# Kernel tuning notes

Hardware: AMD Instinct MI355X
Metric: run time of the kernel (lower is better)

Reference implementation:

```python
import jax, jax.numpy as jnp
import numpy as np
from jax import lax

KERNEL = 3
NUM_ITERS = 10
SMOOTH = 1.0


def _max_pool3d(x):
    # x: (B, 1, Z, Y, X); 3x3x3 max pool, stride 1, SAME padding
    return lax.reduce_window(
        x, -jnp.inf, lax.max,
        window_dimensions=(1, 1, KERNEL, KERNEL, KERNEL),
        window_strides=(1, 1, 1, 1, 1),
        padding='SAME')


def _soft_erode(x):
    return -_max_pool3d(-x)


def _soft_dilate(x):
    return _max_pool3d(x)


def _soft_open(x):
    return _soft_dilate(_soft_erode(x))


def _soft_skeletonize(img):
    skel = jax.nn.relu(img - _soft_open(img))
    for _ in range(NUM_ITERS):
        img = _soft_erode(img)
        delta = jax.nn.relu(img - _soft_open(img))
        skel = skel + jax.nn.relu(delta - skel * delta)
    return skel


def setup_inputs() -> dict:
    key = jax.random.key(0)
    k1, k2 = jax.random.split(key)
    B, C, Z, Y, X = 2, 2, 192, 192, 192
    logits = jax.random.normal(k1, (B, C, Z, Y, X), dtype=jnp.float32)
    targets = jax.random.randint(k2, (B, Z, Y, X), 0, 2, dtype=jnp.int32)
    return {"logits": logits, "targets": targets}


def reference(logits, targets):
    probs = jax.nn.softmax(logits, axis=1)
    pred_surface = probs[:, 1:2]                                  # (B,1,Z,Y,X)
    gt_surface = (targets == 1).astype(jnp.float32)[:, None]      # (B,1,Z,Y,X)
    skel_pred = _soft_skeletonize(pred_surface)
    skel_gt = _soft_skeletonize(gt_surface)
    tprec = (jnp.sum(skel_pred * gt_surface) + SMOOTH) / (jnp.sum(skel_pred) + SMOOTH)
    tsens = (jnp.sum(skel_gt * pred_surface) + SMOOTH) / (jnp.sum(skel_gt) + SMOOTH)
    cl_dice = 2.0 * tprec * tsens / (tprec + tsens + 1e-07)
    return 1.0 - cl_dice
```

## Files before the change

### kernel.cpp

```cpp
#include <hip/hip_runtime.h>
#include <hip/hip_fp16.h>


#define ZD 192
#define YD 192
#define XD 192
constexpr int PLANE = YD * XD;
constexpr int VOL   = ZD * PLANE;
constexpr int NVOL4 = 4 * VOL;

constexpr int XT = 64, YT = 16, ZCH = 16;
constexpr int IWQ = 18, SIW = 19;
constexpr int IH  = 20;
constexpr int NIMGQ = IH * IWQ;
constexpr int BWQ = 17, BH = 18;
constexpr int NBQ  = BH * BWQ;
constexpr int STEPS = ZCH + 4;
#define PINF __builtin_inff()

typedef _Float16 hv2 __attribute__((ext_vector_type(2)));
struct __align__(8) H4 { hv2 lo, hi; };

__device__ __forceinline__ unsigned h2u(hv2 h) { return __builtin_bit_cast(unsigned, h); }
__device__ __forceinline__ hv2 u2h(unsigned u) { return __builtin_bit_cast(hv2, u); }

__device__ __forceinline__ hv2 h2min(hv2 a, hv2 b) {
#if __has_builtin(__builtin_elementwise_min)
    return __builtin_elementwise_min(a, b);
#else
    unsigned r, ua = h2u(a), ub = h2u(b);
    asm("v_pk_min_f16 %0, %1, %2" : "=v"(r) : "v"(ua), "v"(ub));
    return u2h(r);
#endif
}
__device__ __forceinline__ hv2 h2max(hv2 a, hv2 b) {
#if __has_builtin(__builtin_elementwise_max)
    return __builtin_elementwise_max(a, b);
#else
    unsigned r, ua = h2u(a), ub = h2u(b);
    asm("v_pk_max_f16 %0, %1, %2" : "=v"(r) : "v"(ua), "v"(ub));
    return u2h(r);
#endif
}
__device__ __forceinline__ hv2 shf1(hv2 c, hv2 n) {
    return u2h(__builtin_amdgcn_alignbit(h2u(n), h2u(c), 16));
}
__device__ __forceinline__ H4 h4min(H4 a, H4 b) { H4 r; r.lo = h2min(a.lo, b.lo); r.hi = h2min(a.hi, b.hi); return r; }
__device__ __forceinline__ H4 h4max(H4 a, H4 b) { H4 r; r.lo = h2max(a.lo, b.lo); r.hi = h2max(a.hi, b.hi); return r; }
__device__ __forceinline__ H4 pk4(float4 v) {
    H4 r;
    r.lo.x = (_Float16)v.x; r.lo.y = (_Float16)v.y;
    r.hi.x = (_Float16)v.z; r.hi.y = (_Float16)v.w;
    return r;
}
__device__ __forceinline__ H4 ldp4(const __half* p) {
    const uint2 v = *(const uint2*)p;
    H4 r; r.lo = u2h(v.x); r.hi = u2h(v.y); return r;
}
__device__ __forceinline__ void stp4(__half* p, H4 v) {
    uint2 u; u.x = h2u(v.lo); u.y = h2u(v.hi);
    *(uint2*)p = u;
}
__device__ __forceinline__ void sth4(__half* p, float4 v) { stp4(p, pk4(v)); }

template <int MODE>
__global__ __launch_bounds__(256)
void fused_kernel(const __half* __restrict__ a_in,
                  __half* __restrict__ a_out,
                  __half* __restrict__ skel,
                  const float* __restrict__ logits,
                  const int* __restrict__ targets,
                  float* __restrict__ sums)
{
    __shared__ __align__(16) hv2 simg[2][IH * SIW * 2];
    __shared__ __align__(16) hv2 sbp[NBQ * 2 + 4];
    __shared__ float red[4][2];

    const int tx = threadIdx.x, ty = threadIdx.y;
    const int tid = ty * 16 + tx;
    const int x0 = (blockIdx.x % 3) * XT, y0 = (blockIdx.x / 3) * YT;
    const int z0 = blockIdx.y * ZCH;
    const int zf = blockIdx.z;
    const int bb = zf & 1, field = zf >> 1;
    const size_t voff = (size_t)zf * VOL;
    const __half* inb  = a_in  + voff;
    __half*       outb = a_out + voff;
    __half*       skb  = skel  + voff;
    const float* lg0 = logits + (size_t)(bb * 2) * VOL;
    const float* lg1 = lg0 + VOL;
    const int*   tgb = targets + (size_t)bb * VOL;

    const hv2 INF2  = u2h(0x7C007C00u);
    const hv2 NINF2 = u2h(0xFC00FC00u);
    const hv2 Z2    = u2h(0u);
    const H4 HINF4  = { INF2, INF2 };
    const H4 HNINF4 = { NINF2, NINF2 };
    const H4 HZ4    = { Z2, Z2 };

    const int q1off = ((tid & 3) << 6) + (tid >> 2);

    int im_qi[2] = { tid, 256 + q1off };
    int im_addr[2], im_goff[2]; bool im_ok[2], im_has[2];
    #pragma unroll
    for (int j = 0; j < 2; ++j) {
        const int qi = im_qi[j];
        const int r = qi / IWQ, c = qi - r * IWQ;
        const int gy = y0 - 2 + r, gxb = x0 - 4 + 4 * c;
        im_has[j] = (qi < NIMGQ);
        im_ok[j]  = im_has[j] && gy >= 0 && gy < YD && gxb >= 0 && gxb < XD;
        im_goff[j] = gy * XD + gxb;
        im_addr[j] = (r * SIW + c) * 2;
    }
    int bqi[2], brow[2], bcol[2]; bool bhas[2]; H4 bmask[2];
    #pragma unroll
    for (int j = 0; j < 2; ++j) {
        const int qi = (j == 0) ? tid : 256 + q1off;
        bqi[j] = qi;
        bhas[j] = (qi < NBQ);
        const int r = qi / BWQ, c = qi - r * BWQ;
        brow[j] = r; bcol[j] = c;
        const int gy = y0 - 1 + r, gxb = x0 - 1 + 4 * c;
        const bool yv = (gy >= 0 && gy < YD);
        float4 m;
        m.x = (yv && gxb     >= 0 && gxb     < XD) ? PINF : -PINF;
        m.y = (yv && gxb + 1 >= 0 && gxb + 1 < XD) ? PINF : -PINF;
        m.z = (yv && gxb + 2 >= 0 && gxb + 2 < XD) ? PINF : -PINF;
        m.w = (yv && gxb + 3 >= 0 && gxb + 3 < XD) ? PINF : -PINF;
        bmask[j] = pk4(m);
    }

    auto loadq = [&](int zi, int j) -> H4 {
        if (zi < 0 || zi >= ZD || !im_ok[j]) return HINF4;
        const size_t p = (size_t)zi * PLANE + im_goff[j];
        if constexpr (MODE == 0) {
            if (field) {
                const int4 t = *(const int4*)(tgb + p);
                return pk4(make_float4(t.x == 1 ? 1.f : 0.f, t.y == 1 ? 1.f : 0.f,
                                       t.z == 1 ? 1.f : 0.f, t.w == 1 ? 1.f : 0.f));
            } else {
                const float4 a = *(const float4*)(lg0 + p);
                const float4 b = *(const float4*)(lg1 + p);
                return pk4(make_float4(1.f / (1.f + __expf(a.x - b.x)),
                                       1.f / (1.f + __expf(a.y - b.y)),
                                       1.f / (1.f + __expf(a.z - b.z)),
                                       1.f / (1.f + __expf(a.w - b.w))));
            }
        } else {
            return ldp4(inb + p);
        }
    };

    auto s1_of = [&](const hv2* sp, int j) -> H4 {
        const hv2* p = sp + (brow[j] * SIW + bcol[j]) * 2;
        const hv2 A0 = p[1];
        const hv2 A1 = p[SIW * 2 + 1];
        const hv2 A2 = p[SIW * 4 + 1];
        const H4 B0 = *(const H4*)(p + 2);
        const H4 B1 = *(const H4*)(p + SIW * 2 + 2);
        const H4 B2 = *(const H4*)(p + SIW * 4 + 2);
        const hv2 Ah = h2min(A0, h2min(A1, A2));
        const hv2 Bl = h2min(B0.lo, h2min(B1.lo, B2.lo));
        const hv2 Bh = h2min(B0.hi, h2min(B1.hi, B2.hi));
        const hv2 S1 = shf1(Ah, Bl);
        const hv2 S2 = shf1(Bl, Bh);
        H4 r;
        r.lo = h2min(Ah, h2min(S1, Bl));
        r.hi = h2min(Bl, h2min(S2, Bh));
        return r;
    };

    H4 p2a = HINF4, p1a = HINF4;
    H4 p2b = HINF4, p1b = HINF4;
    H4 s2p1 = HNINF4, s2p2 = HNINF4;
    H4 icp1 = HZ4, icp2 = HZ4, bcp1 = HZ4;
    float sd = 0.f, ss = 0.f;

    H4 ca0 = loadq(z0 - 2, 0);
    H4 ca1 = loadq(z0 - 2, 1);

    #pragma unroll 2
    for (int s = 0; s < STEPS; ++s) {
        const int zi = z0 - 2 + s;
        hv2* sp = simg[s & 1];
        *(H4*)&sp[im_addr[0]] = ca0;
        if (im_has[1]) *(H4*)&sp[im_addr[1]] = ca1;
        if (s + 1 < STEPS) { ca0 = loadq(zi + 1, 0); ca1 = loadq(zi + 1, 1); }
        __syncthreads();
        const int zb = zi - 1;
        const bool zbv = (s >= 2) && (zb >= 0) && (zb < ZD);
        {
            const H4 cur = s1_of(sp, 0);
            if (zbv) {
                const H4 b = h4min(h4min(p2a, p1a), cur);
                *(H4*)&sbp[2 * bqi[0]] = h4min(b, bmask[0]);
            }
            p2a = p1a; p1a = cur;
        }
        if (bhas[1]) {
            const H4 cur = s1_of(sp, 1);
            if (zbv) {
                const H4 b = h4min(h4min(p2b, p1b), cur);
                *(H4*)&sbp[2 * bqi[1]] = h4min(b, bmask[1]);
            }
            p2b = p1b; p1b = cur;
        }
        const H4 icq = *(const H4*)&sp[((ty + 2) * SIW + tx + 1) * 2];
        __syncthreads();
        H4 s2n = HNINF4, bcq = HZ4;
        if (zbv) {
            const hv2* p = sbp + (ty * BWQ + tx) * 2;
            const H4 U0 = *(const H4*)p;
            const H4 U1 = *(const H4*)(p + BWQ * 2);
            const H4 U2 = *(const H4*)(p + BWQ * 4);
            const hv2 V0 = p[2];
            const hv2 V1 = p[BWQ * 2 + 2];
            const hv2 V2 = p[BWQ * 4 + 2];
            bcq.lo = shf1(U1.lo, U1.hi);
            bcq.hi = shf1(U1.hi, V1);
            const hv2 Ul = h2max(U0.lo, h2max(U1.lo, U2.lo));
            const hv2 Uh = h2max(U0.hi, h2max(U1.hi, U2.hi));
            const hv2 Vl = h2max(V0, h2max(V1, V2));
            const hv2 S1 = shf1(Ul, Uh);
            const hv2 S2 = shf1(Uh, Vl);
            s2n.lo = h2max(Ul, h2max(S1, Uh));
            s2n.hi = h2max(Uh, h2max(S2, Vl));
        }
        if (s >= 4) {
            const int zo = zi - 2;
            const H4 d = h4max(s2p2, h4max(s2p1, s2n));
            float4 dl;
            dl.x = fmaxf((float)icp2.lo.x - (float)d.lo.x, 0.f);
            dl.y = fmaxf((float)icp2.lo.y - (float)d.lo.y, 0.f);
            dl.z = fmaxf((float)icp2.hi.x - (float)d.hi.x, 0.f);
            dl.w = fmaxf((float)icp2.hi.y - (float)d.hi.y, 0.f);
            const size_t idx = (size_t)zo * PLANE + (size_t)(y0 + ty) * XD + (x0 + 4 * tx);
            if constexpr (MODE == 0) {
                sth4(skb + idx, dl);
                stp4(outb + idx, bcp1);
            } else {
                const H4 sk = ldp4(skb + idx);
                const float s0x = (float)sk.lo.x, s0y = (float)sk.lo.y;
                const float s0z = (float)sk.hi.x, s0w = (float)sk.hi.y;
                float4 sv;
                sv.x = s0x + dl.x * (1.f - s0x);
                sv.y = s0y + dl.y * (1.f - s0y);
                sv.z = s0z + dl.z * (1.f - s0z);
                sv.w = s0w + dl.w * (1.f - s0w);
                if constexpr (MODE == 1) {
                    sth4(skb + idx, sv);
                    stp4(outb + idx, bcp1);
                } else {
                    float4 w;
                    if (field) {
                        const float4 a = *(const float4*)(lg0 + idx);
                        const float4 b = *(const float4*)(lg1 + idx);
                        w = make_float4(1.f / (1.f + __expf(a.x - b.x)),
                                        1.f / (1.f + __expf(a.y - b.y)),
                                        1.f / (1.f + __expf(a.z - b.z)),
                                        1.f / (1.f + __expf(a.w - b.w)));
                    } else {
                        const int4 t = *(const int4*)(tgb + idx);
                        w = make_float4(t.x == 1 ? 1.f : 0.f, t.y == 1 ? 1.f : 0.f,
                                        t.z == 1 ? 1.f : 0.f, t.w == 1 ? 1.f : 0.f);
                    }
                    sd += sv.x * w.x + sv.y * w.y + sv.z * w.z + sv.w * w.w;
                    ss += sv.x + sv.y + sv.z + sv.w;
                }
            }
        }
        s2p2 = s2p1; s2p1 = s2n;
        icp2 = icp1; icp1 = icq;
        bcp1 = bcq;
    }

    if constexpr (MODE == 2) {
        #pragma unroll
        for (int o = 32; o; o >>= 1) {
            sd += __shfl_down(sd, o, 64);
            ss += __shfl_down(ss, o, 64);
        }
        const int w = tid >> 6;
        if ((tid & 63) == 0) { red[w][0] = sd; red[w][1] = ss; }
        __syncthreads();
        if (tid == 0) {
            float a = 0.f, b = 0.f;
            #pragma unroll
            for (int i = 0; i < 4; ++i) { a += red[i][0]; b += red[i][1]; }
            atomicAdd(&sums[2 * field + 0], a);
            atomicAdd(&sums[2 * field + 1], b);
        }
    }
}

__global__ void final_kernel(const float* __restrict__ sums, float* __restrict__ out)
{
    float tprec = (sums[0] + 1.f) / (sums[1] + 1.f);
    float tsens = (sums[2] + 1.f) / (sums[3] + 1.f);
    float cl = 2.f * tprec * tsens / (tprec + tsens + 1e-7f);
    out[0] = 1.f - cl;
}

extern "C" void kernel_launch(void* const* d_in, const int* in_sizes, int n_in,
                              void* d_out, int out_size, void* d_ws, size_t ws_size,
                              hipStream_t stream)
{
    const float* logits  = (const float*)d_in[0];
    const int*   targets = (const int*)d_in[1];
    float* out  = (float*)d_out;

    float*  sums = (float*)d_ws;
    __half* A    = (__half*)(sums + 16);
    __half* B    = A + NVOL4;
    __half* SK   = B + NVOL4;
    __half* bufs[2] = { A, B };

    hipMemsetAsync(sums, 0, 16 * sizeof(float), stream);

    dim3 g(3 * (YD / YT), ZD / ZCH, 4);
    dim3 blk(16, 16, 1);

    fused_kernel<0><<<g, blk, 0, stream>>>(A, A, SK, logits, targets, sums);
    for (int k = 1; k <= 9; ++k) {
        const __half* cin = bufs[(k + 1) & 1];
        __half*       cout = bufs[k & 1];
        fused_kernel<1><<<g, blk, 0, stream>>>(cin, cout, SK, logits, targets, sums);
    }
    fused_kernel<2><<<g, blk, 0, stream>>>(bufs[1], A, SK, logits, targets, sums);

    final_kernel<<<1, 1, 0, stream>>>(sums, out);
}
```

Before: 981.7 us.

## Prefetch next step's skeleton and logits/targets, use LDS-only barriers

Loads of the skeleton value and the logits or targets for the next output plane are issued one iteration early into registers, so global-load latency overlaps the LDS stencil work instead of stalling at the point of use. The two __syncthreads are replaced by a custom barrier that waits only on LDS counters (lgkmcnt) and wraps s_barrier with scheduling fences, so outstanding global loads are not drained at each barrier. This raises register pressure and relies on correct ordering of the prefetch index, which is computed as zi-1 and read at the next step's zo.

```diff
diff --git a/kernel.cpp b/kernel.cpp
--- a/kernel.cpp
+++ b/kernel.cpp
@@ -62,6 +62,13 @@
     *(uint2*)p = u;
 }
 __device__ __forceinline__ void sth4(__half* p, float4 v) { stp4(p, pk4(v)); }
+
+__device__ __forceinline__ void ldsbar() {
+    asm volatile("s_waitcnt lgkmcnt(0)" ::: "memory");
+    __builtin_amdgcn_sched_barrier(0);
+    __builtin_amdgcn_s_barrier();
+    __builtin_amdgcn_sched_barrier(0);
+}
 
 template <int MODE>
 __global__ __launch_bounds__(256)
@@ -175,6 +182,12 @@
     H4 icp1 = HZ4, icp2 = HZ4, bcp1 = HZ4;
     float sd = 0.f, ss = 0.f;
 
+    const size_t eb = (size_t)(y0 + ty) * XD + (x0 + 4 * tx);
+    H4 skpf = HZ4;
+    float4 wapf = make_float4(0.f, 0.f, 0.f, 0.f);
+    float4 wbpf = make_float4(0.f, 0.f, 0.f, 0.f);
+    int4   tpf  = make_int4(0, 0, 0, 0);
+
     H4 ca0 = loadq(z0 - 2, 0);
     H4 ca1 = loadq(z0 - 2, 1);
 
@@ -185,7 +198,7 @@
         *(H4*)&sp[im_addr[0]] = ca0;
         if (im_has[1]) *(H4*)&sp[im_addr[1]] = ca1;
         if (s + 1 < STEPS) { ca0 = loadq(zi + 1, 0); ca1 = loadq(zi + 1, 1); }
-        __syncthreads();
+        ldsbar();
         const int zb = zi - 1;
         const bool zbv = (s >= 2) && (zb >= 0) && (zb < ZD);
         {
@@ -205,7 +218,7 @@
             p2b = p1b; p1b = cur;
         }
         const H4 icq = *(const H4*)&sp[((ty + 2) * SIW + tx + 1) * 2];
-        __syncthreads();
+        ldsbar();
         H4 s2n = HNINF4, bcq = HZ4;
         if (zbv) {
             const hv2* p = sbp + (ty * BWQ + tx) * 2;
@@ -233,12 +246,12 @@
             dl.y = fmaxf((float)icp2.lo.y - (float)d.lo.y, 0.f);
             dl.z = fmaxf((float)icp2.hi.x - (float)d.hi.x, 0.f);
             dl.w = fmaxf((float)icp2.hi.y - (float)d.hi.y, 0.f);
-            const size_t idx = (size_t)zo * PLANE + (size_t)(y0 + ty) * XD + (x0 + 4 * tx);
+            const size_t idx = (size_t)zo * PLANE + eb;
             if constexpr (MODE == 0) {
                 sth4(skb + idx, dl);
                 stp4(outb + idx, bcp1);
             } else {
-                const H4 sk = ldp4(skb + idx);
+                const H4 sk = skpf;
                 const float s0x = (float)sk.lo.x, s0y = (float)sk.lo.y;
                 const float s0z = (float)sk.hi.x, s0w = (float)sk.hi.y;
                 float4 sv;
@@ -252,19 +265,30 @@
                 } else {
                     float4 w;
                     if (field) {
-                        const float4 a = *(const float4*)(lg0 + idx);
-                        const float4 b = *(const float4*)(lg1 + idx);
-                        w = make_float4(1.f / (1.f + __expf(a.x - b.x)),
-                                        1.f / (1.f + __expf(a.y - b.y)),
-                                        1.f / (1.f + __expf(a.z - b.z)),
-                                        1.f / (1.f + __expf(a.w - b.w)));
+                        w = make_float4(1.f / (1.f + __expf(wapf.x - wbpf.x)),
+                                        1.f / (1.f + __expf(wapf.y - wbpf.y)),
+                                        1.f / (1.f + __expf(wapf.z - wbpf.z)),
+                                        1.f / (1.f + __expf(wapf.w - wbpf.w)));
                     } else {
-                        const int4 t = *(const int4*)(tgb + idx);
-                        w = make_float4(t.x == 1 ? 1.f : 0.f, t.y == 1 ? 1.f : 0.f,
-                                        t.z == 1 ? 1.f : 0.f, t.w == 1 ? 1.f : 0.f);
+                        w = make_float4(tpf.x == 1 ? 1.f : 0.f, tpf.y == 1 ? 1.f : 0.f,
+                                        tpf.z == 1 ? 1.f : 0.f, tpf.w == 1 ? 1.f : 0.f);
                     }
                     sd += sv.x * w.x + sv.y * w.y + sv.z * w.z + sv.w * w.w;
                     ss += sv.x + sv.y + sv.z + sv.w;
+                }
+            }
+        }
+        if constexpr (MODE != 0) {
+            if (s >= 3 && s + 1 < STEPS) {
+                const size_t nidx = (size_t)(zi - 1) * PLANE + eb;
+                skpf = ldp4(skb + nidx);
+                if constexpr (MODE == 2) {
+                    if (field) {
+                        wapf = *(const float4*)(lg0 + nidx);
+                        wbpf = *(const float4*)(lg1 + nidx);
+                    } else {
+                        tpf = *(const int4*)(tgb + nidx);
+                    }
                 }
             }
         }
```

Result: slower. 1.013 ms (+3.2%).

## Fuse two skeletonize iterations per kernel with deeper z-halo streaming

Applied to the files above, without the earlier changes.

Adds a fused2p kernel that performs two erode/open/skeleton-update iterations per pass. It carries a wider halo (3 in y and z, 4 in x) and pipelines two erosion stages through shared memory while streaming along z. The launch sequence drops from 11 per-iteration kernels to 5 two-iteration kernels plus the final reduction kernel, roughly halving global reads and writes of the intermediate fp16 volumes and the skeleton. In exchange each block recomputes halo regions, uses more shared memory and registers, and takes more z-steps per chunk, with no double buffering of the input slab.

```diff
diff --git a/kernel.cpp b/kernel.cpp
--- a/kernel.cpp
+++ b/kernel.cpp
@@ -10,12 +10,24 @@
 constexpr int NVOL4 = 4 * VOL;
 
 constexpr int XT = 64, YT = 16, ZCH = 16;
+
+constexpr int AWQ = 18, SA_Q = 19, AH = 22;
+constexpr int NAQ = AH * AWQ;
+constexpr int EWQ = 17, SE_Q = 17;
+constexpr int E1H = 20;
+constexpr int NE1Q = E1H * EWQ;
+constexpr int E2H = 18;
+constexpr int NE2Q = E2H * EWQ;
+constexpr int F2STEPS = ZCH + 8;
+constexpr int SAW2 = SA_Q * 2;
+constexpr int SEW2 = SE_Q * 2;
+
 constexpr int IWQ = 18, SIW = 19;
 constexpr int IH  = 20;
 constexpr int NIMGQ = IH * IWQ;
 constexpr int BWQ = 17, BH = 18;
 constexpr int NBQ  = BH * BWQ;
-constexpr int STEPS = ZCH + 4;
+constexpr int TSTEPS = ZCH + 4;
 #define PINF __builtin_inff()
 
 typedef _Float16 hv2 __attribute__((ext_vector_type(2)));
@@ -62,6 +74,310 @@
     *(uint2*)p = u;
 }
 __device__ __forceinline__ void sth4(__half* p, float4 v) { stp4(p, pk4(v)); }
+
+template <int MODE>
+__global__ __launch_bounds__(256)
+void fused2p_kernel(const __half* __restrict__ a_in,
+                    __half* __restrict__ a_out,
+                    __half* __restrict__ skel,
+                    const float* __restrict__ logits,
+                    const int* __restrict__ targets)
+{
+    __shared__ __align__(16) hv2 sA [AH  * SA_Q * 2];
+    __shared__ __align__(16) hv2 sE1[E1H * SE_Q * 2 + 2];
+    __shared__ __align__(16) hv2 sE2[E2H * SE_Q * 2];
+
+    const int tx = threadIdx.x, ty = threadIdx.y;
+    const int tid = ty * 16 + tx;
+    const int x0 = (blockIdx.x % 3) * XT, y0 = (blockIdx.x / 3) * YT;
+    const int z0 = blockIdx.y * ZCH;
+    const int zf = blockIdx.z;
+    const int bb = zf & 1, field = zf >> 1;
+    const size_t voff = (size_t)zf * VOL;
+    const __half* inb  = a_in  + voff;
+    __half*       outb = a_out + voff;
+    __half*       skb  = skel  + voff;
+    const float* lg0 = logits + (size_t)(bb * 2) * VOL;
+    const float* lg1 = lg0 + VOL;
+    const int*   tgb = targets + (size_t)bb * VOL;
+
+    const hv2 INF2  = u2h(0x7C007C00u);
+    const hv2 NINF2 = u2h(0xFC00FC00u);
+    const hv2 Z2    = u2h(0u);
+    const H4 HINF4  = { INF2, INF2 };
+    const H4 HNINF4 = { NINF2, NINF2 };
+    const H4 HZ4    = { Z2, Z2 };
+    const _Float16 HN1 = (_Float16)(-PINF);
+
+    const int q1off = ((tid & 3) << 6) + (tid >> 2);
+
+    int a_ad[2], a_go[2]; bool a_ok[2], a_h[2];
+    #pragma unroll
+    for (int j = 0; j < 2; ++j) {
+        const int qi = (j == 0) ? tid : 256 + q1off;
+        const int r = qi / AWQ, c = qi - r * AWQ;
+        const int gy = y0 - 3 + r, gxb = x0 - 4 + 4 * c;
+        a_h[j]  = (qi < NAQ);
+        a_ok[j] = a_h[j] && gy >= 0 && gy < YD && gxb >= 0 && gxb < XD;
+        a_go[j] = gy * XD + gxb;
+        a_ad[j] = (r * SA_Q + c) * 2;
+    }
+    int e1st[2], e1rd[2]; bool e1h[2]; H4 e1m[2];
+    #pragma unroll
+    for (int j = 0; j < 2; ++j) {
+        const int qi = (j == 0) ? tid : 256 + q1off;
+        const int r = qi / EWQ, c = qi - r * EWQ;
+        e1h[j]  = (qi < NE1Q);
+        e1st[j] = (r * SE_Q + c) * 2;
+        e1rd[j] = (r * SA_Q + c) * 2;
+        const int gy = y0 - 2 + r, gxb = x0 - 2 + 4 * c;
+        const bool yv = (gy >= 0 && gy < YD);
+        float4 m;
+        m.x = (yv && gxb     >= 0 && gxb     < XD) ? -PINF : PINF;
+        m.y = (yv && gxb + 1 >= 0 && gxb + 1 < XD) ? -PINF : PINF;
+        m.z = (yv && gxb + 2 >= 0 && gxb + 2 < XD) ? -PINF : PINF;
+        m.w = (yv && gxb + 3 >= 0 && gxb + 3 < XD) ? -PINF : PINF;
+        e1m[j] = pk4(m);
+    }
+    int e2st[2], e2rd[2]; bool e2h[2]; H4 e2m[2];
+    #pragma unroll
+    for (int j = 0; j < 2; ++j) {
+        const int qi = (j == 0) ? tid : 256 + q1off;
+        const int r = qi / EWQ, c = qi - r * EWQ;
+        e2h[j]  = (qi < NE2Q);
+        e2st[j] = (r * SE_Q + c) * 2;
+        e2rd[j] = (r * SE_Q + c) * 2;
+        const int gy = y0 - 1 + r, gxb = x0 - 1 + 4 * c;
+        const bool yv = (gy >= 0 && gy < YD);
+        float4 m;
+        m.x = (yv && gxb     >= 0 && gxb     < XD) ? PINF : -PINF;
+        m.y = (yv && gxb + 1 >= 0 && gxb + 1 < XD) ? PINF : -PINF;
+        m.z = (yv && gxb + 2 >= 0 && gxb + 2 < XD) ? PINF : -PINF;
+        m.w = (yv && gxb + 3 >= 0 && gxb + 3 < XD) ? PINF : -PINF;
+        e2m[j] = pk4(m);
+    }
+
+    const int gy0 = y0 + ty, gx0 = x0 + 4 * tx;
+    const bool rok0 = (gy0 > 0), rok2 = (gy0 < YD - 1);
+    const bool lok  = (gx0 > 0), rokx = (gx0 + 4 < XD);
+
+    auto loadq = [&](int zi, int j) -> H4 {
+        if (zi < 0 || zi >= ZD || zi > z0 + ZCH + 2 || !a_ok[j]) return HINF4;
+        const size_t p = (size_t)zi * PLANE + a_go[j];
+        if constexpr (MODE == 0) {
+            if (field) {
+                const int4 t = *(const int4*)(tgb + p);
+                return pk4(make_float4(t.x == 1 ? 1.f : 0.f, t.y == 1 ? 1.f : 0.f,
+                                       t.z == 1 ? 1.f : 0.f, t.w == 1 ? 1.f : 0.f));
+            } else {
+                const float4 a = *(const float4*)(lg0 + p);
+                const float4 b = *(const float4*)(lg1 + p);
+                return pk4(make_float4(1.f / (1.f + __expf(a.x - b.x)),
+                                       1.f / (1.f + __expf(a.y - b.y)),
+                                       1.f / (1.f + __expf(a.z - b.z)),
+                                       1.f / (1.f + __expf(a.w - b.w))));
+            }
+        } else {
+            return ldp4(inb + p);
+        }
+    };
+
+    auto s1p = [&](int j) -> H4 {
+        const hv2* p = sA + e1rd[j];
+        const H4 A0 = *(const H4*)p;
+        const H4 B0 = *(const H4*)(p + 2);
+        const H4 A1 = *(const H4*)(p + SAW2);
+        const H4 B1 = *(const H4*)(p + SAW2 + 2);
+        const H4 A2 = *(const H4*)(p + 2 * SAW2);
+        const H4 B2 = *(const H4*)(p + 2 * SAW2 + 2);
+        const hv2 Al = h2min(A0.lo, h2min(A1.lo, A2.lo));
+        const hv2 Ah = h2min(A0.hi, h2min(A1.hi, A2.hi));
+        const hv2 Bl = h2min(B0.lo, h2min(B1.lo, B2.lo));
+        const hv2 Bh = h2min(B0.hi, h2min(B1.hi, B2.hi));
+        const hv2 M1 = shf1(Al, Ah);
+        const hv2 M2 = shf1(Ah, Bl);
+        const hv2 M3 = shf1(Bl, Bh);
+        H4 r;
+        r.lo = h2min(M1, h2min(Ah, M2));
+        r.hi = h2min(M2, h2min(Bl, M3));
+        return r;
+    };
+    auto s2p = [&](int j) -> H4 {
+        const hv2* p = sE1 + e2rd[j];
+        const H4 E0 = *(const H4*)p;
+        const hv2 F0 = p[2];
+        const H4 E1 = *(const H4*)(p + SEW2);
+        const hv2 F1 = p[SEW2 + 2];
+        const H4 E2 = *(const H4*)(p + 2 * SEW2);
+        const hv2 F2 = p[2 * SEW2 + 2];
+        const hv2 El = h2min(E0.lo, h2min(E1.lo, E2.lo));
+        const hv2 Eh = h2min(E0.hi, h2min(E1.hi, E2.hi));
+        const hv2 Fl = h2min(F0, h2min(F1, F2));
+        const hv2 M1 = shf1(El, Eh);
+        const hv2 M2 = shf1(Eh, Fl);
+        H4 r;
+        r.lo = h2min(El, h2min(M1, Eh));
+        r.hi = h2min(Eh, h2min(M2, Fl));
+        return r;
+    };
+
+    H4 s1p2a = HINF4, s1p1a = HINF4, s1p2b = HINF4, s1p1b = HINF4;
+    H4 s2p2a = HINF4, s2p1a = HINF4, s2p2b = HINF4, s2p1b = HINF4;
+    H4 xm1p2 = HNINF4, xm1p1 = HNINF4;
+    H4 xm2p2 = HNINF4, xm2p1 = HNINF4;
+    H4 e1w0 = HINF4, e1w1 = HINF4, e2w0 = HINF4, e2w1 = HINF4;
+    H4 icp1 = HZ4, icp2 = HZ4, icp3 = HZ4;
+    H4 ec1 = HZ4, ec2 = HZ4, ec3 = HZ4;
+    H4 e2cp = HZ4;
+    H4 dl1r1 = HZ4, dl1r2 = HZ4;
+
+    const size_t eb = (size_t)gy0 * XD + gx0;
+
+    H4 ca0 = loadq(z0 - 3, 0);
+    H4 ca1 = loadq(z0 - 3, 1);
+
+    #pragma unroll 1
+    for (int s = 0; s < F2STEPS; ++s) {
+        const int z = z0 - 3 + s;
+        *(H4*)&sA[a_ad[0]] = ca0;
+        if (a_h[1]) *(H4*)&sA[a_ad[1]] = ca1;
+        if (s >= 1) {
+            *(H4*)&sE1[e1st[0]] = h4max(e1w0, e1m[0]);
+            if (e1h[1]) *(H4*)&sE1[e1st[1]] = h4max(e1w1, e1m[1]);
+        }
+        if (s >= 2) {
+            *(H4*)&sE2[e2st[0]] = h4min(e2w0, e2m[0]);
+            if (e2h[1]) *(H4*)&sE2[e2st[1]] = h4min(e2w1, e2m[1]);
+        }
+        __syncthreads();
+
+        if (s + 1 < F2STEPS) { ca0 = loadq(z + 1, 0); ca1 = loadq(z + 1, 1); }
+
+        {
+            const H4 cur = s1p(0);
+            e1w0 = h4min(s1p2a, h4min(s1p1a, cur));
+            s1p2a = s1p1a; s1p1a = cur;
+        }
+        if (e1h[1]) {
+            const H4 cur = s1p(1);
+            e1w1 = h4min(s1p2b, h4min(s1p1b, cur));
+            s1p2b = s1p1b; s1p1b = cur;
+        }
+
+        const int  ze1 = z - 2;
+        const bool ve1 = (s >= 1) && (ze1 >= 0) && (ze1 < ZD);
+
+        {
+            const H4 cur = ve1 ? s2p(0) : HINF4;
+            e2w0 = h4min(s2p2a, h4min(s2p1a, cur));
+            s2p2a = s2p1a; s2p1a = cur;
+        }
+        if (e2h[1]) {
+            const H4 cur = ve1 ? s2p(1) : HINF4;
+            e2w1 = h4min(s2p2b, h4min(s2p1b, cur));
+            s2p2b = s2p1b; s2p1b = cur;
+        }
+
+        H4 xm1c = HNINF4, e1cc = HZ4;
+        if (ve1) {
+            const hv2* p = sE1 + ((ty + 1) * SE_Q + tx) * 2;
+            H4 A0 = *(const H4*)p;
+            H4 Bq0 = *(const H4*)(p + 2);
+            const H4 A1 = *(const H4*)(p + SEW2);
+            const H4 Bq1 = *(const H4*)(p + SEW2 + 2);
+            H4 A2 = *(const H4*)(p + 2 * SEW2);
+            H4 Bq2 = *(const H4*)(p + 2 * SEW2 + 2);
+            e1cc.lo = A1.hi;
+            e1cc.hi = Bq1.lo;
+            if (!rok0) { A0 = HNINF4; Bq0 = HNINF4; }
+            if (!rok2) { A2 = HNINF4; Bq2 = HNINF4; }
+            const hv2 Al = h2max(A0.lo, h2max(A1.lo, A2.lo));
+            const hv2 Ah = h2max(A0.hi, h2max(A1.hi, A2.hi));
+            const hv2 Bl = h2max(Bq0.lo, h2max(Bq1.lo, Bq2.lo));
+            const hv2 Bh = h2max(Bq0.hi, h2max(Bq1.hi, Bq2.hi));
+            hv2 M1 = shf1(Al, Ah);
+            const hv2 M2 = shf1(Ah, Bl);
+            hv2 M3 = shf1(Bl, Bh);
+            if (!lok)  M1.x = HN1;
+            if (!rokx) M3.y = HN1;
+            xm1c.lo = h2max(M1, h2max(Ah, M2));
+            xm1c.hi = h2max(M2, h2max(Bl, M3));
+        }
+        const H4 d1v = h4max(xm1p2, h4max(xm1p1, xm1c));
+        xm1p2 = xm1p1; xm1p1 = xm1c;
+
+        const int  ze2 = z - 4;
+        const bool ve2 = (s >= 2) && (ze2 >= 0) && (ze2 < ZD);
+        H4 xm2c = HNINF4, e2cc = HZ4;
+        if (ve2) {
+            const hv2* p = sE2 + (ty * SE_Q + tx) * 2;
+            const H4 U0 = *(const H4*)p;
+            const hv2 V0 = p[2];
+            const H4 U1 = *(const H4*)(p + SEW2);
+            const hv2 V1 = p[SEW2 + 2];
+            const H4 U2 = *(const H4*)(p + 2 * SEW2);
+            const hv2 V2 = p[2 * SEW2 + 2];
+            e2cc.lo = shf1(U1.lo, U1.hi);
+            e2cc.hi = shf1(U1.hi, V1);
+            const hv2 Ul = h2max(U0.lo, h2max(U1.lo, U2.lo));
+            const hv2 Uh = h2max(U0.hi, h2max(U1.hi, U2.hi));
+            const hv2 Vl = h2max(V0, h2max(V1, V2));
+            const hv2 M1 = shf1(Ul, Uh);
+            const hv2 M2 = shf1(Uh, Vl);
+            xm2c.lo = h2max(Ul, h2max(M1, Uh));
+            xm2c.hi = h2max(Uh, h2max(M2, Vl));
+        }
+        const H4 d2v = h4max(xm2p2, h4max(xm2p1, xm2c));
+        xm2p2 = xm2p1; xm2p1 = xm2c;
+
+        const H4 icq = *(const H4*)&sA[((ty + 3) * SA_Q + tx + 1) * 2];
+
+        float4 dl1n, dl2;
+        dl1n.x = fmaxf((float)icp3.lo.x - (float)d1v.lo.x, 0.f);
+        dl1n.y = fmaxf((float)icp3.lo.y - (float)d1v.lo.y, 0.f);
+        dl1n.z = fmaxf((float)icp3.hi.x - (float)d1v.hi.x, 0.f);
+        dl1n.w = fmaxf((float)icp3.hi.y - (float)d1v.hi.y, 0.f);
+        dl2.x = fmaxf((float)ec3.lo.x - (float)d2v.lo.x, 0.f);
+        dl2.y = fmaxf((float)ec3.lo.y - (float)d2v.lo.y, 0.f);
+        dl2.z = fmaxf((float)ec3.hi.x - (float)d2v.hi.x, 0.f);
+        dl2.w = fmaxf((float)ec3.hi.y - (float)d2v.hi.y, 0.f);
+        const H4 dA = dl1r2;
+        const H4 av = e2cp;
+
+        __syncthreads();
+
+        if (s >= 8) {
+            const int zo = z - 5;
+            const size_t idx = (size_t)zo * PLANE + eb;
+            float4 sk;
+            const float dAx = (float)dA.lo.x, dAy = (float)dA.lo.y;
+            const float dAz = (float)dA.hi.x, dAw = (float)dA.hi.y;
+            if constexpr (MODE == 0) {
+                sk = make_float4(dAx, dAy, dAz, dAw);
+            } else {
+                const H4 s0 = ldp4(skb + idx);
+                const float s0x = (float)s0.lo.x, s0y = (float)s0.lo.y;
+                const float s0z = (float)s0.hi.x, s0w = (float)s0.hi.y;
+                sk.x = s0x + dAx * (1.f - s0x);
+                sk.y = s0y + dAy * (1.f - s0y);
+                sk.z = s0z + dAz * (1.f - s0z);
+                sk.w = s0w + dAw * (1.f - s0w);
+            }
+            float4 sv;
+            sv.x = sk.x + dl2.x * (1.f - sk.x);
+            sv.y = sk.y + dl2.y * (1.f - sk.y);
+            sv.z = sk.z + dl2.z * (1.f - sk.z);
+            sv.w = sk.w + dl2.w * (1.f - sk.w);
+            sth4(skb + idx, sv);
+            stp4(outb + idx, av);
+        }
+
+        dl1r2 = dl1r1; dl1r1 = pk4(dl1n);
+        icp3 = icp2; icp2 = icp1; icp1 = icq;
+        ec3 = ec2; ec2 = ec1; ec1 = e1cc;
+        e2cp = e2cc;
+    }
+}
 
 template <int MODE>
 __global__ __launch_bounds__(256)
@@ -84,7 +400,6 @@
     const int bb = zf & 1, field = zf >> 1;
     const size_t voff = (size_t)zf * VOL;
     const __half* inb  = a_in  + voff;
-    __half*       outb = a_out + voff;
     __half*       skb  = skel  + voff;
     const float* lg0 = logits + (size_t)(bb * 2) * VOL;
     const float* lg1 = lg0 + VOL;
@@ -132,22 +447,7 @@
     auto loadq = [&](int zi, int j) -> H4 {
         if (zi < 0 || zi >= ZD || !im_ok[j]) return HINF4;
         const size_t p = (size_t)zi * PLANE + im_goff[j];
-        if constexpr (MODE == 0) {
-            if (field) {
-                const int4 t = *(const int4*)(tgb + p);
-                return pk4(make_float4(t.x == 1 ? 1.f : 0.f, t.y == 1 ? 1.f : 0.f,
-                                       t.z == 1 ? 1.f : 0.f, t.w == 1 ? 1.f : 0.f));
-            } else {
-                const float4 a = *(const float4*)(lg0 + p);
-                const float4 b = *(const float4*)(lg1 + p);
-                return pk4(make_float4(1.f / (1.f + __expf(a.x - b.x)),
-                                       1.f / (1.f + __expf(a.y - b.y)),
-                                       1.f / (1.f + __expf(a.z - b.z)),
-                                       1.f / (1.f + __expf(a.w - b.w))));
-            }
-        } else {
-            return ldp4(inb + p);
-        }
+        return ldp4(inb + p);
     };
 
     auto s1_of = [&](const hv2* sp, int j) -> H4 {
@@ -172,19 +472,19 @@
     H4 p2a = HINF4, p1a = HINF4;
     H4 p2b = HINF4, p1b = HINF4;
     H4 s2p1 = HNINF4, s2p2 = HNINF4;
-    H4 icp1 = HZ4, icp2 = HZ4, bcp1 = HZ4;
+    H4 icp1 = HZ4, icp2 = HZ4;
     float sd = 0.f, ss = 0.f;
 
     H4 ca0 = loadq(z0 - 2, 0);
     H4 ca1 = loadq(z0 - 2, 1);
 
     #pragma unroll 2
-    for (int s = 0; s < STEPS; ++s) {
+    for (int s = 0; s < TSTEPS; ++s) {
         const int zi = z0 - 2 + s;
         hv2* sp = simg[s & 1];
         *(H4*)&sp[im_addr[0]] = ca0;
         if (im_has[1]) *(H4*)&sp[im_addr[1]] = ca1;
-        if (s + 1 < STEPS) { ca0 = loadq(zi + 1, 0); ca1 = loadq(zi + 1, 1); }
+        if (s + 1 < TSTEPS) { ca0 = loadq(zi + 1, 0); ca1 = loadq(zi + 1, 1); }
         __syncthreads();
         const int zb = zi - 1;
         const bool zbv = (s >= 2) && (zb >= 0) && (zb < ZD);
@@ -206,7 +506,7 @@
         }
         const H4 icq = *(const H4*)&sp[((ty + 2) * SIW + tx + 1) * 2];
         __syncthreads();
-        H4 s2n = HNINF4, bcq = HZ4;
+        H4 s2n = HNINF4;
         if (zbv) {
             const hv2* p = sbp + (ty * BWQ + tx) * 2;
             const H4 U0 = *(const H4*)p;
@@ -215,8 +515,6 @@
             const hv2 V0 = p[2];
             const hv2 V1 = p[BWQ * 2 + 2];
             const hv2 V2 = p[BWQ * 4 + 2];
-            bcq.lo = shf1(U1.lo, U1.hi);
-            bcq.hi = shf1(U1.hi, V1);
             const hv2 Ul = h2max(U0.lo, h2max(U1.lo, U2.lo));
             const hv2 Uh = h2max(U0.hi, h2max(U1.hi, U2.hi));
             const hv2 Vl = h2max(V0, h2max(V1, V2));
@@ -234,43 +532,32 @@
             dl.z = fmaxf((float)icp2.hi.x - (float)d.hi.x, 0.f);
             dl.w = fmaxf((float)icp2.hi.y - (float)d.hi.y, 0.f);
             const size_t idx = (size_t)zo * PLANE + (size_t)(y0 + ty) * XD + (x0 + 4 * tx);
-            if constexpr (MODE == 0) {
-                sth4(skb + idx, dl);
-                stp4(outb + idx, bcp1);
+            const H4 sk = ldp4(skb + idx);
+            const float s0x = (float)sk.lo.x, s0y = (float)sk.lo.y;
+            const float s0z = (float)sk.hi.x, s0w = (float)sk.hi.y;
+            float4 sv;
+            sv.x = s0x + dl.x * (1.f - s0x);
+            sv.y = s0y + dl.y * (1.f - s0y);
+            sv.z = s0z + dl.z * (1.f - s0z);
+            sv.w = s0w + dl.w * (1.f - s0w);
+            float4 w;
+            if (field) {
+                const float4 a = *(const float4*)(lg0 + idx);
+                const float4 b = *(const float4*)(lg1 + idx);
+                w = make_float4(1.f / (1.f + __expf(a.x - b.x)),
+                                1.f / (1.f + __expf(a.y - b.y)),
+                                1.f / (1.f + __expf(a.z - b.z)),
+                                1.f / (1.f + __expf(a.w - b.w)));
             } else {
-                const H4 sk = ldp4(skb + idx);
-                const float s0x = (float)sk.lo.x, s0y = (float)sk.lo.y;
-                const float s0z = (float)sk.hi.x, s0w = (float)sk.hi.y;
-                float4 sv;
-                sv.x = s0x + dl.x * (1.f - s0x);
-                sv.y = s0y + dl.y * (1.f - s0y);
-                sv.z = s0z + dl.z * (1.f - s0z);
-                sv.w = s0w + dl.w * (1.f - s0w);
-                if constexpr (MODE == 1) {
-                    sth4(skb + idx, sv);
-                    stp4(outb + idx, bcp1);
-                } else {
-                    float4 w;
-                    if (field) {
-                        const float4 a = *(const float4*)(lg0 + idx);
-                        const float4 b = *(const float4*)(lg1 + idx);
-                        w = make_float4(1.f / (1.f + __expf(a.x - b.x)),
-                                        1.f / (1.f + __expf(a.y - b.y)),
-                                        1.f / (1.f + __expf(a.z - b.z)),
-                                        1.f / (1.f + __expf(a.w - b.w)));
-                    } else {
-                        const int4 t = *(const int4*)(tgb + idx);
-                        w = make_float4(t.x == 1 ? 1.f : 0.f, t.y == 1 ? 1.f : 0.f,
-                                        t.z == 1 ? 1.f : 0.f, t.w == 1 ? 1.f : 0.f);
-                    }
-                    sd += sv.x * w.x + sv.y * w.y + sv.z * w.z + sv.w * w.w;
-                    ss += sv.x + sv.y + sv.z + sv.w;
-                }
+                const int4 t = *(const int4*)(tgb + idx);
+                w = make_float4(t.x == 1 ? 1.f : 0.f, t.y == 1 ? 1.f : 0.f,
+                                t.z == 1 ? 1.f : 0.f, t.w == 1 ? 1.f : 0.f);
             }
+            sd += sv.x * w.x + sv.y * w.y + sv.z * w.z + sv.w * w.w;
+            ss += sv.x + sv.y + sv.z + sv.w;
         }
         s2p2 = s2p1; s2p1 = s2n;
         icp2 = icp1; icp1 = icq;
-        bcp1 = bcq;
     }
 
     if constexpr (MODE == 2) {
@@ -312,20 +599,18 @@
     __half* A    = (__half*)(sums + 16);
     __half* B    = A + NVOL4;
     __half* SK   = B + NVOL4;
-    __half* bufs[2] = { A, B };
 
     hipMemsetAsync(sums, 0, 16 * sizeof(float), stream);
 
     dim3 g(3 * (YD / YT), ZD / ZCH, 4);
     dim3 blk(16, 16, 1);
 
-    fused_kernel<0><<<g, blk, 0, stream>>>(A, A, SK, logits, targets, sums);
-    for (int k = 1; k <= 9; ++k) {
-        const __half* cin = bufs[(k + 1) & 1];
-        __half*       cout = bufs[k & 1];
-        fused_kernel<1><<<g, blk, 0, stream>>>(cin, cout, SK, logits, targets, sums);
-    }
-    fused_kernel<2><<<g, blk, 0, stream>>>(bufs[1], A, SK, logits, targets, sums);
+    fused2p_kernel<0><<<g, blk, 0, stream>>>(A, A, SK, logits, targets);
+    fused2p_kernel<1><<<g, blk, 0, stream>>>(A, B, SK, logits, targets);
+    fused2p_kernel<1><<<g, blk, 0, stream>>>(B, A, SK, logits, targets);
+    fused2p_kernel<1><<<g, blk, 0, stream>>>(A, B, SK, logits, targets);
+    fused2p_kernel<1><<<g, blk, 0, stream>>>(B, A, SK, logits, targets);
+    fused_kernel<2><<<g, blk, 0, stream>>>(A, B, SK, logits, targets, sums);
 
     final_kernel<<<1, 1, 0, stream>>>(sums, out);
 }
```

Result: faster. 919.5 us (-6.3%).
